# Kernel optimization log

Measured on AMD Instinct MI355X. Metric: run time of the kernel, lower is better.

## Reference

```python
import jax
import jax.numpy as jnp
from jax import lax
import numpy as np

# Module constants (from init_kwargs)
SCALE = 2
CIN = 256
COUT = 256
KER = 3
R = 4
CMID = CIN // R
PAD = KER // 2          # ConvTranspose2d padding
OUT_PAD = SCALE - 1     # ConvTranspose2d output_padding

B, H, W = 4, 64, 64
HO, WO = H * SCALE, W * SCALE


def conv_transpose2d(x, w, b, stride, padding, output_padding):
    """PyTorch ConvTranspose2d. x: [B,Cin,H,W], w: [Cin,Cout,k,k] (torch layout)."""
    k = w.shape[2]
    # rot180 + swap in/out channels -> regular conv kernel [Cout,Cin,k,k]
    wr = jnp.transpose(jnp.flip(w, (2, 3)), (1, 0, 2, 3))
    pad = (k - 1 - padding, k - 1 - padding + output_padding)
    y = lax.conv_general_dilated(
        x, wr, window_strides=(1, 1), padding=[pad, pad],
        lhs_dilation=(stride, stride),
        dimension_numbers=('NCHW', 'OIHW', 'NCHW'))
    return y + b[None, :, None, None]


def setup_inputs() -> dict:
    key = jax.random.key(0)
    k1, k2, k3, k4, k5 = jax.random.split(key, 5)
    inx = jax.random.normal(k1, (B, CIN, H, W), dtype=jnp.float32)
    mask = jax.random.bernoulli(k2, 0.5, (B, 1, HO, WO)).astype(jnp.float32)
    inv_mask = 1.0 - mask
    # params, initialized per the module's init scheme
    w_high = 0.001 * jax.random.normal(k3, (CIN, COUT, KER, KER), dtype=jnp.float32)
    b_high = jnp.zeros((COUT,), dtype=jnp.float32)
    std1 = float(np.sqrt(2.0 / (CMID * 1 * 1)))
    w_low1 = std1 * jax.random.normal(k4, (CMID, CIN, 1, 1), dtype=jnp.float32)
    b_low1 = jnp.zeros((CMID,), dtype=jnp.float32)
    w_low2 = 0.001 * jax.random.normal(k5, (CMID, COUT, KER, KER), dtype=jnp.float32)
    b_low2 = jnp.zeros((COUT,), dtype=jnp.float32)
    return {"inx": inx, "mask": mask, "inv_mask": inv_mask,
            "w_high": w_high, "b_high": b_high,
            "w_low1": w_low1, "b_low1": b_low1,
            "w_low2": w_low2, "b_low2": b_low2}


def reference(inx, mask, inv_mask, w_high, b_high, w_low1, b_low1, w_low2, b_low2):
    # high branch: full-rank transposed conv, routed by mask
    x1 = conv_transpose2d(inx, w_high, b_high, SCALE, PAD, OUT_PAD) * mask
    # low branch: 1x1 bottleneck then transposed conv, routed by inv_mask
    x2 = jnp.einsum('bchw,oc->bohw', inx, w_low1[:, :, 0, 0]) + b_low1[None, :, None, None]
    x2 = conv_transpose2d(x2, w_low2, b_low2, SCALE, PAD, OUT_PAD) * inv_mask
    return x1 + x2
```

## Files before the change

### kernel.cpp

```cpp
#include <hip/hip_runtime.h>
#include <cstdint>
#include <cstddef>

#define CIN   256
#define COUT  256
#define CMID  64
#define H     64
#define W     64
#define HO    128
#define WO    128
#define BATCH 4

typedef unsigned short u16;
typedef unsigned int   u32;
typedef __attribute__((ext_vector_type(8))) __bf16 bf16x8;
typedef __attribute__((ext_vector_type(4))) float f32x4;

#define XT_ROW  16640
#define X2_ROW  4160

#define AS1 __attribute__((address_space(1)))
#define AS3 __attribute__((address_space(3)))

__device__ __forceinline__ void g2l16(const void* g, const void* l) {
    __builtin_amdgcn_global_load_lds((const AS1 u32*)(uintptr_t)g,
                                     (AS3 u32*)(u32)(uintptr_t)l, 16, 0, 0);
}

__device__ __forceinline__ u16 f2bf(float f) {
    u32 u = __builtin_bit_cast(u32, f);
    u += 0x7fffu + ((u >> 16) & 1u);
    return (u16)(u >> 16);
}

__global__ __launch_bounds__(256) void k_prep(const float* __restrict__ inx,
                                              const float* __restrict__ w1,
                                              const float* __restrict__ b1,
                                              const float* __restrict__ wH,
                                              const float* __restrict__ wL,
                                              u16* __restrict__ Xt,
                                              u16* __restrict__ X2t,
                                              u16* __restrict__ WPH,
                                              u16* __restrict__ WPL) {
    __shared__ u16 sX[32 * 64 * 8];
    __shared__ u16 sW1[8 * 4 * 64 * 8];
    const int blk = blockIdx.x;
    const int tid = threadIdx.x;

    if (blk >= BATCH * 65) {
        const int pb = blk - BATCH * 65;
        const int t = pb / 8;
        const int kc = pb % 8;
        const int co = tid;
        #pragma unroll
        for (int q = 0; q < 4; ++q) {
            u16 pk[8];
            #pragma unroll
            for (int j = 0; j < 8; ++j) {
                int ci = kc * 32 + q * 8 + j;
                pk[j] = f2bf(wH[((size_t)ci * COUT + co) * 9 + t]);
            }
            *(uint4*)(WPH + ((((size_t)t * 8 + kc) * 4 + q) * 256 + co) * 8) = *(uint4*)pk;
        }
        if (kc < 2) {
            #pragma unroll
            for (int q = 0; q < 4; ++q) {
                u16 pk[8];
                #pragma unroll
                for (int j = 0; j < 8; ++j) {
                    int cm = kc * 32 + q * 8 + j;
                    pk[j] = f2bf(wL[((size_t)cm * COUT + co) * 9 + t]);
                }
                *(uint4*)(WPL + ((((size_t)t * 2 + kc) * 4 + q) * 256 + co) * 8) = *(uint4*)pk;
            }
        }
        return;
    }

    const int b = blk / 65;
    const int y = blk % 65;
    u16* xrow  = Xt  + (size_t)(b * 65 + y) * XT_ROW;
    u16* x2row = X2t + (size_t)(b * 65 + y) * X2_ROW;
    if (y == H) {
        uint4 z = {0, 0, 0, 0};
        for (int i = tid; i < XT_ROW / 8; i += 256) *(uint4*)(xrow + i * 8) = z;
        for (int i = tid; i < X2_ROW / 8; i += 256) *(uint4*)(x2row + i * 8) = z;
        return;
    }

    #pragma unroll
    for (int i = 0; i < 16; ++i) {
        int lin4 = i * 256 + tid;
        float4 v = ((const float4*)w1)[lin4];
        int lin = lin4 * 4;
        int cm = lin >> 8, ci = lin & 255;
        u16* dp = sW1 + (((size_t)(ci >> 3) * 64 + cm) * 8) + (ci & 7);
        dp[0] = f2bf(v.x); dp[1] = f2bf(v.y); dp[2] = f2bf(v.z); dp[3] = f2bf(v.w);
    }

    const int x = tid & 63, g0 = tid >> 6;
    #pragma unroll
    for (int gg = 0; gg < 8; ++gg) {
        const int s = gg * 4 + g0;
        u16 pk[8];
        #pragma unroll
        for (int j = 0; j < 8; ++j)
            pk[j] = f2bf(inx[(((size_t)b * CIN + s * 8 + j) * H + y) * W + x]);
        uint4 v = *(uint4*)pk;
        *(uint4*)(xrow + ((size_t)s * 65 + x) * 8) = v;
        *(uint4*)(sX   + ((size_t)s * 64 + x) * 8) = v;
    }
    if (tid < 32) {
        uint4 z = {0, 0, 0, 0};
        *(uint4*)(xrow + ((size_t)tid * 65 + 64) * 8) = z;
    }
    if (tid < 8) {
        uint4 z = {0, 0, 0, 0};
        *(uint4*)(x2row + ((size_t)tid * 65 + 64) * 8) = z;
    }
    __syncthreads();

    const int wv = tid >> 6, lane = tid & 63, l15 = lane & 15, q = lane >> 4;
    f32x4 acc[4] = {};
    #pragma unroll
    for (int kc = 0; kc < 8; ++kc) {
        bf16x8 bfr = *(const bf16x8*)(sX + ((size_t)(kc * 4 + q) * 64 + wv * 16 + l15) * 8);
        #pragma unroll
        for (int mi = 0; mi < 4; ++mi) {
            bf16x8 af = *(const bf16x8*)(sW1 + (((size_t)kc * 4 + q) * 64 + mi * 16 + l15) * 8);
            acc[mi] = __builtin_amdgcn_mfma_f32_16x16x32_bf16(af, bfr, acc[mi], 0, 0, 0);
        }
    }
    const int xx = wv * 16 + l15;
    #pragma unroll
    for (int mi = 0; mi < 4; ++mi) {
        const int s = mi * 2 + (q >> 1);
        u16 pk[4];
        #pragma unroll
        for (int r = 0; r < 4; ++r)
            pk[r] = f2bf(acc[mi][r] + b1[mi * 16 + q * 4 + r]);
        *(ushort4*)(x2row + ((size_t)s * 65 + xx) * 8 + (q & 1) * 4) = *(ushort4*)&pk[0];
    }
}

#define SA_G 1536
#define SB_G 520

template<int NR>
struct Step {
    __device__ static constexpr int count() { return NR * 10; }
    __device__ static bool hi(int c) { return c < NR * 8; }
    __device__ static int  kc(int c) { int cc = hi(c) ? c : c - NR * 8; return NR == 1 ? cc : cc >> 1; }
    __device__ static int  dy(int c) { int cc = hi(c) ? c : c - NR * 8; return NR == 1 ? 0 : (cc & 1); }
    __device__ static int  ky(int c) { return NR == 1 ? 1 : (dy(c) ? 0 : 2); }
};

template<int NR>
__device__ __forceinline__ void stage(int c, u16* sAb, u16* sBb,
                                      const u16* __restrict__ Xt,
                                      const u16* __restrict__ X2t,
                                      const u16* __restrict__ WPH,
                                      const u16* __restrict__ WPL,
                                      int b, int y0, int coH, int wid, int lane) {
    const bool hi = Step<NR>::hi(c);
    const int kc = Step<NR>::kc(c);
    const int dy = Step<NR>::dy(c);
    const int ky = Step<NR>::ky(c);
    const int kcn = hi ? 8 : 2;
    const u16* Wp = hi ? WPH : WPL;
    const u16* Xp = hi ? Xt : X2t;
    const size_t rowStr = hi ? XT_ROW : X2_ROW;
    #pragma unroll
    for (int i = 0; i < 6; ++i) {
        const int seg = i * 4 + wid;
        const int kx = seg >> 3, qq = (seg >> 1) & 3, h = seg & 1;
        const u16* src = Wp + ((((size_t)(ky * 3 + kx) * kcn + kc) * 4 + qq) * 256
                                + coH * 128 + h * 64 + lane) * 8;
        g2l16(src, sAb + ((size_t)((kx * 4 + qq) * 128 + h * 64)) * 8);
    }
    #pragma unroll
    for (int i = 0; i < 2; ++i) {
        const u16* src = Xp + (size_t)(b * 65 + y0 + dy + i) * rowStr
                            + ((size_t)(kc * 4 + wid) * 65 + lane) * 8;
        g2l16(src, sBb + ((size_t)(i * 4 + wid) * 65) * 8);
    }
}

template<int NR>
__device__ __forceinline__ void compute(int c, const u16* sAb, const u16* sBb,
                                        int rowR, int coQ, int q, int l15,
                                        const int* __restrict__ selE,
                                        const int* __restrict__ selO,
                                        f32x4 ce[4][4], f32x4 co_[4][4]) {
    const bool hi = Step<NR>::hi(c);
    const bf16x8 z8 = {};
    const u16* bp = sBb + (((size_t)(rowR * 4 + q)) * 65 + l15) * 8;
    bf16x8 be[4], bo0[4], bo1[4];
    #pragma unroll
    for (int ni = 0; ni < 4; ++ni) {
        bf16x8 b0 = *(const bf16x8*)(bp + ni * 128);
        bf16x8 b1 = *(const bf16x8*)(bp + ni * 128 + 8);
        const bool kE = hi ? (selE[ni] != 0) : (selE[ni] == 0);
        const bool kO = hi ? (selO[ni] != 0) : (selO[ni] == 0);
        be[ni]  = kE ? b0 : z8;
        bo0[ni] = kO ? b0 : z8;
        bo1[ni] = kO ? b1 : z8;
    }
    const u16* ap = sAb + ((size_t)(q * 128 + coQ * 64 + l15)) * 8;
    #pragma unroll
    for (int mi = 0; mi < 4; ++mi) {
        bf16x8 a = *(const bf16x8*)(ap + (1 * 512 + mi * 16) * 8);
        #pragma unroll
        for (int ni = 0; ni < 4; ++ni)
            ce[mi][ni] = __builtin_amdgcn_mfma_f32_16x16x32_bf16(a, be[ni], ce[mi][ni], 0, 0, 0);
    }
    #pragma unroll
    for (int mi = 0; mi < 4; ++mi) {
        bf16x8 a = *(const bf16x8*)(ap + (2 * 512 + mi * 16) * 8);
        #pragma unroll
        for (int ni = 0; ni < 4; ++ni)
            co_[mi][ni] = __builtin_amdgcn_mfma_f32_16x16x32_bf16(a, bo0[ni], co_[mi][ni], 0, 0, 0);
    }
    #pragma unroll
    for (int mi = 0; mi < 4; ++mi) {
        bf16x8 a = *(const bf16x8*)(ap + (mi * 16) * 8);
        #pragma unroll
        for (int ni = 0; ni < 4; ++ni)
            co_[mi][ni] = __builtin_amdgcn_mfma_f32_16x16x32_bf16(a, bo1[ni], co_[mi][ni], 0, 0, 0);
    }
}

__global__ __launch_bounds__(256, 2) void k_main(const u16* __restrict__ Xt,
                                                 const u16* __restrict__ X2t,
                                                 const u16* __restrict__ WPH,
                                                 const u16* __restrict__ WPL,
                                                 const float* __restrict__ bH,
                                                 const float* __restrict__ bL,
                                                 const float* __restrict__ mask,
                                                 float* __restrict__ out) {
    __shared__ u16 sA[2][SA_G * 8];
    __shared__ u16 sB[2][SB_G * 8];

    const int blk = blockIdx.x;
    const int coH = blk & 1;
    const int yP  = (blk >> 1) & 31;
    const int b   = (blk >> 6) & 3;
    const int py  = blk >> 8;
    const int y0  = yP * 2;

    const int tid = threadIdx.x;
    const int wid = tid >> 6, lane = tid & 63, l15 = lane & 15, q = lane >> 4;
    const int rowR = wid >> 1, coQ = wid & 1;
    const int oy = 2 * (y0 + rowR) + py;

    int selE[4], selO[4];
    const float* mrow = mask + ((size_t)b * HO + oy) * WO;
    #pragma unroll
    for (int ni = 0; ni < 4; ++ni) {
        float2 mm = *(const float2*)(mrow + 2 * (ni * 16 + l15));
        selE[ni] = (mm.x != 0.f);
        selO[ni] = (mm.y != 0.f);
    }

    if (tid < 16) {
        uint4 z = {0, 0, 0, 0};
        *(uint4*)(sB[tid >> 3] + (((size_t)(tid & 7)) * 65 + 64) * 8) = z;
    }

    f32x4 ce[4][4] = {}, co_[4][4] = {};

    if (py == 0) {
        constexpr int NS = Step<1>::count();
        stage<1>(0, sA[0], sB[0], Xt, X2t, WPH, WPL, b, y0, coH, wid, lane);
        __syncthreads();
        #pragma unroll
        for (int c = 0; c < NS; ++c) {
            if (c + 1 < NS)
                stage<1>(c + 1, sA[(c + 1) & 1], sB[(c + 1) & 1],
                         Xt, X2t, WPH, WPL, b, y0, coH, wid, lane);
            compute<1>(c, sA[c & 1], sB[c & 1], rowR, coQ, q, l15, selE, selO, ce, co_);
            __syncthreads();
        }
    } else {
        constexpr int NS = Step<2>::count();
        stage<2>(0, sA[0], sB[0], Xt, X2t, WPH, WPL, b, y0, coH, wid, lane);
        __syncthreads();
        #pragma unroll
        for (int c = 0; c < NS; ++c) {
            if (c + 1 < NS)
                stage<2>(c + 1, sA[(c + 1) & 1], sB[(c + 1) & 1],
                         Xt, X2t, WPH, WPL, b, y0, coH, wid, lane);
            compute<2>(c, sA[c & 1], sB[c & 1], rowR, coQ, q, l15, selE, selO, ce, co_);
            __syncthreads();
        }
    }

    #pragma unroll
    for (int mi = 0; mi < 4; ++mi) {
        const int cob = coH * 128 + coQ * 64 + mi * 16 + q * 4;
        float bh[4], bl[4];
        #pragma unroll
        for (int r = 0; r < 4; ++r) { bh[r] = bH[cob + r]; bl[r] = bL[cob + r]; }
        #pragma unroll
        for (int r = 0; r < 4; ++r) {
            float* orow = out + (((size_t)b * COUT + cob + r) * HO + oy) * WO;
            #pragma unroll
            for (int ni = 0; ni < 4; ++ni) {
                const int x = ni * 16 + l15;
                float2 v;
                v.x = ce[mi][ni][r]  + (selE[ni] ? bh[r] : bl[r]);
                v.y = co_[mi][ni][r] + (selO[ni] ? bh[r] : bl[r]);
                *(float2*)(orow + 2 * x) = v;
            }
        }
    }
}

extern "C" void kernel_launch(void* const* d_in, const int* in_sizes, int n_in,
                              void* d_out, int out_size, void* d_ws, size_t ws_size,
                              hipStream_t stream) {
    const float* inx    = (const float*)d_in[0];
    const float* mask   = (const float*)d_in[1];
    const float* w_high = (const float*)d_in[3];
    const float* b_high = (const float*)d_in[4];
    const float* w_low1 = (const float*)d_in[5];
    const float* b_low1 = (const float*)d_in[6];
    const float* w_low2 = (const float*)d_in[7];
    const float* b_low2 = (const float*)d_in[8];
    float* out = (float*)d_out;

    char* ws = (char*)d_ws;
    u16* Xt  = (u16*)(ws);
    u16* X2t = (u16*)(ws + 8652800);
    u16* WPH = (u16*)(ws + 10816000);
    u16* WPL = (u16*)(ws + 11995648);

    k_prep<<<BATCH * 65 + 72, 256, 0, stream>>>(inx, w_low1, b_low1, w_high, w_low2,
                                                Xt, X2t, WPH, WPL);
    k_main<<<512, 256, 0, stream>>>(Xt, X2t, WPH, WPL, b_high, b_low2, mask, out);
}
```

Baseline: 125.7 us.

## Compact mask-routed pixels into per-branch lists to skip zeroed MFMA work

```diff
diff --git a/kernel.cpp b/kernel.cpp
--- a/kernel.cpp
+++ b/kernel.cpp
@@ -149,10 +149,10 @@
 template<int NR>
 struct Step {
     __device__ static constexpr int count() { return NR * 10; }
-    __device__ static bool hi(int c) { return c < NR * 8; }
-    __device__ static int  kc(int c) { int cc = hi(c) ? c : c - NR * 8; return NR == 1 ? cc : cc >> 1; }
-    __device__ static int  dy(int c) { int cc = hi(c) ? c : c - NR * 8; return NR == 1 ? 0 : (cc & 1); }
-    __device__ static int  ky(int c) { return NR == 1 ? 1 : (dy(c) ? 0 : 2); }
+    __device__ static constexpr bool hi(int c) { return c < NR * 8; }
+    __device__ static constexpr int  kc(int c) { int cc = hi(c) ? c : c - NR * 8; return NR == 1 ? cc : cc >> 1; }
+    __device__ static constexpr int  dy(int c) { int cc = hi(c) ? c : c - NR * 8; return NR == 1 ? 0 : (cc & 1); }
+    __device__ static constexpr int  ky(int c) { return NR == 1 ? 1 : (dy(c) ? 0 : 2); }
 };
 
 template<int NR>
@@ -187,46 +187,151 @@
 }
 
 template<int NR>
-__device__ __forceinline__ void compute(int c, const u16* sAb, const u16* sBb,
-                                        int rowR, int coQ, int q, int l15,
-                                        const int* __restrict__ selE,
-                                        const int* __restrict__ selO,
-                                        f32x4 ce[4][4], f32x4 co_[4][4]) {
-    const bool hi = Step<NR>::hi(c);
-    const bf16x8 z8 = {};
-    const u16* bp = sBb + (((size_t)(rowR * 4 + q)) * 65 + l15) * 8;
-    bf16x8 be[4], bo0[4], bo1[4];
-    #pragma unroll
-    for (int ni = 0; ni < 4; ++ni) {
-        bf16x8 b0 = *(const bf16x8*)(bp + ni * 128);
-        bf16x8 b1 = *(const bf16x8*)(bp + ni * 128 + 8);
-        const bool kE = hi ? (selE[ni] != 0) : (selE[ni] == 0);
-        const bool kO = hi ? (selO[ni] != 0) : (selO[ni] == 0);
-        be[ni]  = kE ? b0 : z8;
-        bo0[ni] = kO ? b0 : z8;
-        bo1[ni] = kO ? b1 : z8;
-    }
-    const u16* ap = sAb + ((size_t)(q * 128 + coQ * 64 + l15)) * 8;
+__device__ __forceinline__ void run_main(const u16* __restrict__ Xt,
+                                         const u16* __restrict__ X2t,
+                                         const u16* __restrict__ WPH,
+                                         const u16* __restrict__ WPL,
+                                         const float* __restrict__ bH,
+                                         const float* __restrict__ bL,
+                                         const float* __restrict__ mask,
+                                         float* __restrict__ out,
+                                         u16* sA, u16* sB,
+                                         u16* sList, u32* sCnt,
+                                         int b, int y0, int py, int coH) {
+    const int tid = threadIdx.x;
+    const int wid = tid >> 6, lane = tid & 63, l15 = lane & 15, q = lane >> 4;
+    const int rowR = wid >> 1, coQ = wid & 1;
+    const int oy = 2 * (y0 + rowR) + py;
+    constexpr int NS = Step<NR>::count();
+
+    stage<NR>(0, sA, sB, Xt, X2t, WPH, WPL, b, y0, coH, wid, lane);
+    __syncthreads();
+
+    {
+        const int row = wid >> 1, par = wid & 1;
+        const int oyw = 2 * (y0 + row) + py;
+        const float mv = mask[((size_t)b * HO + oyw) * WO + 2 * lane + par];
+        const bool m = (mv != 0.f);
+        unsigned long long bal = __ballot(m);
+        u32 cnt = (u32)__popcll(bal);
+        u32 below = __builtin_amdgcn_mbcnt_hi((u32)(bal >> 32),
+                      __builtin_amdgcn_mbcnt_lo((u32)bal, 0));
+        u32 teh = (cnt + 15) >> 4;
+        u32 pos = m ? below : teh * 16 + ((u32)lane - below);
+        sList[(row * 2 + par) * 80 + pos] = (u16)lane;
+        if (lane == 0) sCnt[row * 2 + par] = cnt;
+    }
+    __syncthreads();
+
+    const int baseRQ = (rowR * 4 + q) * 65;
+    const u32 cntE = sCnt[rowR * 2 + 0];
+    const u32 cntO = sCnt[rowR * 2 + 1];
+    const int tHE = __builtin_amdgcn_readfirstlane((cntE + 15) >> 4);
+    const int tTE = __builtin_amdgcn_readfirstlane(((cntE + 15) >> 4) + ((64 - cntE + 15) >> 4));
+    const int tHO = __builtin_amdgcn_readfirstlane((cntO + 15) >> 4);
+    const int tTO = __builtin_amdgcn_readfirstlane(((cntO + 15) >> 4) + ((64 - cntO + 15) >> 4));
+    int offE[5], offO2[5], offO0[5];
+    #pragma unroll
+    for (int t = 0; t < 5; ++t) {
+        const u16 eE = sList[(rowR * 2 + 0) * 80 + t * 16 + l15];
+        const u16 eO = sList[(rowR * 2 + 1) * 80 + t * 16 + l15];
+        const int ixE = (eE == 0xFFFF) ? 64 : (int)eE;
+        const int ix2 = (eO == 0xFFFF) ? 64 : (int)eO;
+        const int ix0 = (eO == 0xFFFF) ? 64 : (int)eO + 1;
+        offE[t]  = (baseRQ + ixE) * 8;
+        offO2[t] = (baseRQ + ix2) * 8;
+        offO0[t] = (baseRQ + ix0) * 8;
+    }
+
+    f32x4 accE[5][4] = {}, accO[5][4] = {};
+
+    #pragma unroll
+    for (int c = 0; c < NS; ++c) {
+        if (c + 1 < NS)
+            stage<NR>(c + 1, sA + ((c + 1) & 1) * (SA_G * 8), sB + ((c + 1) & 1) * (SB_G * 8),
+                      Xt, X2t, WPH, WPL, b, y0, coH, wid, lane);
+        {
+            const u16* sAb = sA + (c & 1) * (SA_G * 8);
+            const u16* sBb = sB + (c & 1) * (SB_G * 8);
+            const u16* ap = sAb + ((size_t)(q * 128 + coQ * 64 + l15)) * 8;
+            {
+                bf16x8 aE[4];
+                #pragma unroll
+                for (int mi = 0; mi < 4; ++mi)
+                    aE[mi] = *(const bf16x8*)(ap + (512 + mi * 16) * 8);
+                const int t0 = Step<NR>::hi(c) ? 0 : tHE;
+                const int t1 = Step<NR>::hi(c) ? tHE : tTE;
+                #pragma unroll
+                for (int t = 0; t < 5; ++t) {
+                    if (t >= t0 && t < t1) {
+                        bf16x8 bf = *(const bf16x8*)(sBb + offE[t]);
+                        #pragma unroll
+                        for (int mi = 0; mi < 4; ++mi)
+                            accE[t][mi] = __builtin_amdgcn_mfma_f32_16x16x32_bf16(
+                                aE[mi], bf, accE[t][mi], 0, 0, 0);
+                    }
+                }
+            }
+            {
+                bf16x8 a2[4], a0[4];
+                #pragma unroll
+                for (int mi = 0; mi < 4; ++mi) {
+                    a2[mi] = *(const bf16x8*)(ap + (1024 + mi * 16) * 8);
+                    a0[mi] = *(const bf16x8*)(ap + (mi * 16) * 8);
+                }
+                const int t0 = Step<NR>::hi(c) ? 0 : tHO;
+                const int t1 = Step<NR>::hi(c) ? tHO : tTO;
+                #pragma unroll
+                for (int t = 0; t < 5; ++t) {
+                    if (t >= t0 && t < t1) {
+                        bf16x8 b2 = *(const bf16x8*)(sBb + offO2[t]);
+                        bf16x8 b0 = *(const bf16x8*)(sBb + offO0[t]);
+                        #pragma unroll
+                        for (int mi = 0; mi < 4; ++mi)
+                            accO[t][mi] = __builtin_amdgcn_mfma_f32_16x16x32_bf16(
+                                a2[mi], b2, accO[t][mi], 0, 0, 0);
+                        #pragma unroll
+                        for (int mi = 0; mi < 4; ++mi)
+                            accO[t][mi] = __builtin_amdgcn_mfma_f32_16x16x32_bf16(
+                                a0[mi], b0, accO[t][mi], 0, 0, 0);
+                    }
+                }
+            }
+        }
+        __syncthreads();
+    }
+
     #pragma unroll
     for (int mi = 0; mi < 4; ++mi) {
-        bf16x8 a = *(const bf16x8*)(ap + (1 * 512 + mi * 16) * 8);
-        #pragma unroll
-        for (int ni = 0; ni < 4; ++ni)
-            ce[mi][ni] = __builtin_amdgcn_mfma_f32_16x16x32_bf16(a, be[ni], ce[mi][ni], 0, 0, 0);
-    }
-    #pragma unroll
-    for (int mi = 0; mi < 4; ++mi) {
-        bf16x8 a = *(const bf16x8*)(ap + (2 * 512 + mi * 16) * 8);
-        #pragma unroll
-        for (int ni = 0; ni < 4; ++ni)
-            co_[mi][ni] = __builtin_amdgcn_mfma_f32_16x16x32_bf16(a, bo0[ni], co_[mi][ni], 0, 0, 0);
-    }
-    #pragma unroll
-    for (int mi = 0; mi < 4; ++mi) {
-        bf16x8 a = *(const bf16x8*)(ap + (mi * 16) * 8);
-        #pragma unroll
-        for (int ni = 0; ni < 4; ++ni)
-            co_[mi][ni] = __builtin_amdgcn_mfma_f32_16x16x32_bf16(a, bo1[ni], co_[mi][ni], 0, 0, 0);
+        const int cob = coH * 128 + coQ * 64 + mi * 16 + q * 4;
+        float bh[4], bl[4];
+        #pragma unroll
+        for (int r = 0; r < 4; ++r) { bh[r] = bH[cob + r]; bl[r] = bL[cob + r]; }
+        #pragma unroll
+        for (int t = 0; t < 5; ++t) {
+            if (t < tTE) {
+                const bool isH = t < tHE;
+                const int ixE = offE[t] / 8 - baseRQ;
+                if (ixE < 64) {
+                    const int ox = 2 * ixE;
+                    #pragma unroll
+                    for (int r = 0; r < 4; ++r)
+                        out[(((size_t)(b * COUT + cob + r)) * HO + oy) * WO + ox] =
+                            accE[t][mi][r] + (isH ? bh[r] : bl[r]);
+                }
+            }
+            if (t < tTO) {
+                const bool isH = t < tHO;
+                const int ix2 = offO2[t] / 8 - baseRQ;
+                if (ix2 < 64) {
+                    const int ox = 2 * ix2 + 1;
+                    #pragma unroll
+                    for (int r = 0; r < 4; ++r)
+                        out[(((size_t)(b * COUT + cob + r)) * HO + oy) * WO + ox] =
+                            accO[t][mi][r] + (isH ? bh[r] : bl[r]);
+                }
+            }
+        }
     }
 }
 
@@ -240,6 +345,8 @@
                                                  float* __restrict__ out) {
     __shared__ u16 sA[2][SA_G * 8];
     __shared__ u16 sB[2][SB_G * 8];
+    __shared__ u16 sList[4 * 80];
+    __shared__ u32 sCnt[4];
 
     const int blk = blockIdx.x;
     const int coH = blk & 1;
@@ -247,73 +354,20 @@
     const int b   = (blk >> 6) & 3;
     const int py  = blk >> 8;
     const int y0  = yP * 2;
-
     const int tid = threadIdx.x;
-    const int wid = tid >> 6, lane = tid & 63, l15 = lane & 15, q = lane >> 4;
-    const int rowR = wid >> 1, coQ = wid & 1;
-    const int oy = 2 * (y0 + rowR) + py;
-
-    int selE[4], selO[4];
-    const float* mrow = mask + ((size_t)b * HO + oy) * WO;
-    #pragma unroll
-    for (int ni = 0; ni < 4; ++ni) {
-        float2 mm = *(const float2*)(mrow + 2 * (ni * 16 + l15));
-        selE[ni] = (mm.x != 0.f);
-        selO[ni] = (mm.y != 0.f);
-    }
 
     if (tid < 16) {
         uint4 z = {0, 0, 0, 0};
         *(uint4*)(sB[tid >> 3] + (((size_t)(tid & 7)) * 65 + 64) * 8) = z;
     }
-
-    f32x4 ce[4][4] = {}, co_[4][4] = {};
-
-    if (py == 0) {
-        constexpr int NS = Step<1>::count();
-        stage<1>(0, sA[0], sB[0], Xt, X2t, WPH, WPL, b, y0, coH, wid, lane);
-        __syncthreads();
-        #pragma unroll
-        for (int c = 0; c < NS; ++c) {
-            if (c + 1 < NS)
-                stage<1>(c + 1, sA[(c + 1) & 1], sB[(c + 1) & 1],
-                         Xt, X2t, WPH, WPL, b, y0, coH, wid, lane);
-            compute<1>(c, sA[c & 1], sB[c & 1], rowR, coQ, q, l15, selE, selO, ce, co_);
-            __syncthreads();
-        }
-    } else {
-        constexpr int NS = Step<2>::count();
-        stage<2>(0, sA[0], sB[0], Xt, X2t, WPH, WPL, b, y0, coH, wid, lane);
-        __syncthreads();
-        #pragma unroll
-        for (int c = 0; c < NS; ++c) {
-            if (c + 1 < NS)
-                stage<2>(c + 1, sA[(c + 1) & 1], sB[(c + 1) & 1],
-                         Xt, X2t, WPH, WPL, b, y0, coH, wid, lane);
-            compute<2>(c, sA[c & 1], sB[c & 1], rowR, coQ, q, l15, selE, selO, ce, co_);
-            __syncthreads();
-        }
-    }
-
-    #pragma unroll
-    for (int mi = 0; mi < 4; ++mi) {
-        const int cob = coH * 128 + coQ * 64 + mi * 16 + q * 4;
-        float bh[4], bl[4];
-        #pragma unroll
-        for (int r = 0; r < 4; ++r) { bh[r] = bH[cob + r]; bl[r] = bL[cob + r]; }
-        #pragma unroll
-        for (int r = 0; r < 4; ++r) {
-            float* orow = out + (((size_t)b * COUT + cob + r) * HO + oy) * WO;
-            #pragma unroll
-            for (int ni = 0; ni < 4; ++ni) {
-                const int x = ni * 16 + l15;
-                float2 v;
-                v.x = ce[mi][ni][r]  + (selE[ni] ? bh[r] : bl[r]);
-                v.y = co_[mi][ni][r] + (selO[ni] ? bh[r] : bl[r]);
-                *(float2*)(orow + 2 * x) = v;
-            }
-        }
-    }
+    if (tid < 160) ((u32*)sList)[tid] = 0xFFFFFFFFu;
+
+    if (py == 0)
+        run_main<1>(Xt, X2t, WPH, WPL, bH, bL, mask, out,
+                    &sA[0][0], &sB[0][0], sList, sCnt, b, y0, py, coH);
+    else
+        run_main<2>(Xt, X2t, WPH, WPL, bH, bL, mask, out,
+                    &sA[0][0], &sB[0][0], sList, sCnt, b, y0, py, coH);
 }
 
 extern "C" void kernel_launch(void* const* d_in, const int* in_sizes, int n_in,
```

New measurement: 140.6 us. 1.12x slower.
